# Performance work log

Measured on AMD Instinct MI355X. Metric: run time of the kernel, lower is better.

Reference implementation:

```python
import jax, jax.numpy as jnp
import numpy as np

N_NODES = 50000
NEG_SLOPE = 0.2


def gatv2_layer(x, src, dst, Wl, bl, Wr, br, att, bias, n_nodes):
    """GATv2Conv (PyG semantics, share_weights=False, concat=True).
    src/dst already include self-loops. att: [H, C]."""
    H, C = att.shape
    xl = (x @ Wl + bl).reshape(n_nodes, H, C)  # source transform
    xr = (x @ Wr + br).reshape(n_nodes, H, C)  # target transform
    # per-edge attention logits: att . LeakyReLU(xl[j] + xr[i])
    g = jax.nn.leaky_relu(xl[src] + xr[dst], NEG_SLOPE)      # [E,H,C]
    score = jnp.einsum('ehc,hc->eh', g, att)                  # [E,H]
    # segment softmax over incoming edges of each dst node
    m = jax.ops.segment_max(score, dst, num_segments=n_nodes)
    ex = jnp.exp(score - m[dst])
    denom = jax.ops.segment_sum(ex, dst, num_segments=n_nodes)
    alpha = ex / denom[dst]                                   # [E,H]
    out = jax.ops.segment_sum(alpha[:, :, None] * xl[src], dst, num_segments=n_nodes)
    return out.reshape(n_nodes, H * C) + bias


def setup_inputs() -> dict:
    key = jax.random.key(0)
    ks = jax.random.split(key, 20)
    N, IN, HID, H, OUT = N_NODES, 128, 64, 4, 64
    E, EL = 800000, 200000

    def w(k, shape, fan_in):
        return jax.random.normal(k, shape, jnp.float32) * (1.0 / np.sqrt(fan_in))

    inp = {
        'x': jax.random.normal(ks[0], (N, IN), jnp.float32),
        'edge_index': jax.random.randint(ks[1], (2, E), 0, N, jnp.int32),
        'edge_label_index': jax.random.randint(ks[2], (2, EL), 0, N, jnp.int32),
        # conv1: in -> hid, heads=4
        'W1l': w(ks[3], (IN, H * HID), IN), 'b1l': jnp.zeros((H * HID,), jnp.float32),
        'W1r': w(ks[4], (IN, H * HID), IN), 'b1r': jnp.zeros((H * HID,), jnp.float32),
        'att1': w(ks[5], (H, HID), HID),   'bias1': jnp.zeros((H * HID,), jnp.float32),
        # conv2: hid*heads -> out, heads=1
        'W2l': w(ks[6], (H * HID, OUT), H * HID), 'b2l': jnp.zeros((OUT,), jnp.float32),
        'W2r': w(ks[7], (H * HID, OUT), H * HID), 'b2r': jnp.zeros((OUT,), jnp.float32),
        'att2': w(ks[8], (1, OUT), OUT),          'bias2': jnp.zeros((OUT,), jnp.float32),
        # mlp decoder: 2*out -> hid -> 1
        'Wm1': w(ks[9], (2 * OUT, HID), 2 * OUT), 'bm1': jnp.zeros((HID,), jnp.float32),
        'Wm2': w(ks[10], (HID, 1), HID),          'bm2': jnp.zeros((1,), jnp.float32),
    }
    return inp


def reference(x, edge_index, edge_label_index,
              W1l, b1l, W1r, b1r, att1, bias1,
              W2l, b2l, W2r, b2r, att2, bias2,
              Wm1, bm1, Wm2, bm2):
    N = x.shape[0]
    # PyG GATv2Conv add_self_loops=True (default)
    loop = jnp.arange(N, dtype=edge_index.dtype)
    src = jnp.concatenate([edge_index[0], loop])
    dst = jnp.concatenate([edge_index[1], loop])

    z = gatv2_layer(x, src, dst, W1l, b1l, W1r, b1r, att1, bias1, N)
    z = jax.nn.relu(z)
    # dropout is identity in eval mode
    z = gatv2_layer(z, src, dst, W2l, b2l, W2r, b2r, att2, bias2, N)

    # decode: gather endpoints, concat, 2-layer MLP -> [EL]
    feat = jnp.concatenate([z[edge_label_index[0]], z[edge_label_index[1]]], axis=-1)
    h = jax.nn.relu(feat @ Wm1 + bm1)
    return (h @ Wm2 + bm2).reshape(-1)
```

## Files before the change

kernel.cpp:

```cpp
#include <hip/hip_runtime.h>
#include <hip/hip_bf16.h>

#define IN_DIM 128
#define HID    64
#define NH     4
#define F1     256
#define OUTD   64
#define NEG    0.2f
#define LOG2E  1.44269504088896f

#define EXP2F(x) __builtin_amdgcn_exp2f(x)

typedef __attribute__((ext_vector_type(8))) short bf16x8;
typedef __attribute__((ext_vector_type(4))) float f32x4;
typedef __attribute__((ext_vector_type(4))) unsigned short u16x4;

__device__ __forceinline__ float bf2f(unsigned short h) {
  return __uint_as_float((unsigned)h << 16);
}
__device__ __forceinline__ unsigned short f2bf(float f) {
  unsigned u = __float_as_uint(f);
  u += 0x7fffu + ((u >> 16) & 1u);
  return (unsigned short)(u >> 16);
}
__device__ __forceinline__ bf16x8 f2bf8(const float* p) {
  float4 lo = *(const float4*)p;
  float4 hi = *(const float4*)(p + 4);
  bf16x8 r;
  r[0] = (short)f2bf(lo.x); r[1] = (short)f2bf(lo.y);
  r[2] = (short)f2bf(lo.z); r[3] = (short)f2bf(lo.w);
  r[4] = (short)f2bf(hi.x); r[5] = (short)f2bf(hi.y);
  r[6] = (short)f2bf(hi.z); r[7] = (short)f2bf(hi.w);
  return r;
}

__global__ __launch_bounds__(256) void k_cvt_all(
    const float* __restrict__ x, unsigned short* __restrict__ xb, int NX8,
    const float* __restrict__ W1l, const float* __restrict__ W1r,
    const float* __restrict__ W2l, const float* __restrict__ W2r,
    const float* __restrict__ Wm1,
    unsigned short* __restrict__ Wt, unsigned short* __restrict__ Wt2,
    unsigned short* __restrict__ Wuv, int* __restrict__ cnt4, int N) {
  int idx = blockIdx.x * 256 + threadIdx.x;
  if (idx < NX8) {
    bf16x8 r = f2bf8(x + (size_t)idx * 8);
    *(bf16x8*)(xb + (size_t)idx * 8) = r;
    return;
  }
  int j0 = idx - NX8;
  if (j0 < 4 * N) cnt4[j0] = 0;
  if (j0 < 512 * IN_DIM) {
    int c = j0 >> 7, k = j0 & 127;
    float v = (c < F1) ? W1l[k * F1 + c] : W1r[k * F1 + (c - F1)];
    Wt[j0] = f2bf(v);
  } else if (j0 < 512 * IN_DIM + 128 * F1) {
    int j = j0 - 512 * IN_DIM;
    int c = j >> 8, k = j & 255;
    float v = (c < OUTD) ? W2l[k * OUTD + c] : W2r[k * OUTD + (c - OUTD)];
    Wt2[j] = f2bf(v);
  } else if (j0 < 512 * IN_DIM + 128 * F1 + 128 * OUTD) {
    int j = j0 - 512 * IN_DIM - 128 * F1;
    int c = j >> 6, k = j & 63;
    float v = (c < OUTD) ? Wm1[k * OUTD + c] : Wm1[(64 + k) * OUTD + (c - OUTD)];
    Wuv[j] = f2bf(v);
  }
}

#define LWS 132
__global__ __launch_bounds__(256) void k_gemm1_mfma(
    const unsigned short* __restrict__ xb, const unsigned short* __restrict__ Wt,
    const float* __restrict__ bl, const float* __restrict__ br,
    unsigned short* __restrict__ xlh, unsigned short* __restrict__ xrh,
    const int* __restrict__ ei, int E, int* __restrict__ cnt4,
    int* __restrict__ rank, int N) {
  __shared__ __align__(16) unsigned short lw[128 * LWS];
  int tid = threadIdx.x, lane = tid & 63, w = tid >> 6;
  int node0 = blockIdx.x * 64 + w * 16;
  int colbase = blockIdx.y * 128;
  int l16 = lane & 15, khi = lane >> 4;
  int koff = khi * 8;
  {
    const unsigned short* src = Wt + (size_t)colbase * IN_DIM;
#pragma unroll
    for (int it = 0; it < 8; it++) {
      int c = it * 256 + tid;
      int col = c >> 4, k8 = (c & 15) * 8;
      *(bf16x8*)(&lw[col * LWS + k8]) = *(const bf16x8*)(src + col * IN_DIM + k8);
    }
  }
  int arow = node0 + l16; if (arow >= N) arow = N - 1;
  const unsigned short* ap = xb + (size_t)arow * IN_DIM + koff;
  bf16x8 b0 = *(const bf16x8*)(ap);
  bf16x8 b1 = *(const bf16x8*)(ap + 32);
  bf16x8 b2 = *(const bf16x8*)(ap + 64);
  bf16x8 b3 = *(const bf16x8*)(ap + 96);
  {
    int gid = blockIdx.y * gridDim.x + blockIdx.x;
    int e = gid * 256 + tid;
    if (e < E) {
      int d = ei[E + e];
      rank[e] = atomicAdd(&cnt4[blockIdx.y * N + d], 1);
    }
  }
  __syncthreads();
  int node = node0 + l16;
  bool nok = node < N;
  bool isL = (colbase < F1);
  unsigned short* dst = isL ? xlh : xrh;
  const float* bias = isL ? bl : br;
  int cofs = isL ? colbase : (colbase - F1);
#pragma unroll
  for (int cp = 0; cp < 4; cp++) {
    int ct0 = cp * 2, ct1 = cp * 2 + 1;
    const unsigned short* wp0 = &lw[(ct0 * 16 + l16) * LWS + koff];
    const unsigned short* wp1 = &lw[(ct1 * 16 + l16) * LWS + koff];
    f32x4 a0 = {0.f, 0.f, 0.f, 0.f};
    f32x4 a1 = {0.f, 0.f, 0.f, 0.f};
    a0 = __builtin_amdgcn_mfma_f32_16x16x32_bf16(*(const bf16x8*)(wp0), b0, a0, 0, 0, 0);
    a1 = __builtin_amdgcn_mfma_f32_16x16x32_bf16(*(const bf16x8*)(wp1), b0, a1, 0, 0, 0);
    a0 = __builtin_amdgcn_mfma_f32_16x16x32_bf16(*(const bf16x8*)(wp0 + 32), b1, a0, 0, 0, 0);
    a1 = __builtin_amdgcn_mfma_f32_16x16x32_bf16(*(const bf16x8*)(wp1 + 32), b1, a1, 0, 0, 0);
    a0 = __builtin_amdgcn_mfma_f32_16x16x32_bf16(*(const bf16x8*)(wp0 + 64), b2, a0, 0, 0, 0);
    a1 = __builtin_amdgcn_mfma_f32_16x16x32_bf16(*(const bf16x8*)(wp1 + 64), b2, a1, 0, 0, 0);
    a0 = __builtin_amdgcn_mfma_f32_16x16x32_bf16(*(const bf16x8*)(wp0 + 96), b3, a0, 0, 0, 0);
    a1 = __builtin_amdgcn_mfma_f32_16x16x32_bf16(*(const bf16x8*)(wp1 + 96), b3, a1, 0, 0, 0);
    int lc0 = ct0 * 16 + khi * 4;
    int lc1 = ct1 * 16 + khi * 4;
    float4 bb0 = *(const float4*)(bias + cofs + lc0);
    float4 bb1 = *(const float4*)(bias + cofs + lc1);
    if (nok) {
      u16x4 o0, o1;
      o0[0] = f2bf(a0[0] + bb0.x); o0[1] = f2bf(a0[1] + bb0.y);
      o0[2] = f2bf(a0[2] + bb0.z); o0[3] = f2bf(a0[3] + bb0.w);
      o1[0] = f2bf(a1[0] + bb1.x); o1[1] = f2bf(a1[1] + bb1.y);
      o1[2] = f2bf(a1[2] + bb1.z); o1[3] = f2bf(a1[3] + bb1.w);
      __builtin_nontemporal_store(o0, (u16x4*)(dst + (size_t)node * F1 + cofs + lc0));
      __builtin_nontemporal_store(o1, (u16x4*)(dst + (size_t)node * F1 + cofs + lc1));
    }
  }
}

__global__ __launch_bounds__(256) void k_gemm2_mfma(
    const unsigned short* __restrict__ zh, const unsigned short* __restrict__ Wt2,
    const float* __restrict__ bl, const float* __restrict__ br,
    unsigned short* __restrict__ xl2h, unsigned short* __restrict__ xr2h, int N) {
  int tid = threadIdx.x, lane = tid & 63, w = tid >> 6;
  int node0 = blockIdx.x * 64 + w * 16;
  int l16 = lane & 15, khi = lane >> 4;
  int koff = khi * 8;
  int arow = node0 + l16; if (arow >= N) arow = N - 1;
  const unsigned short* zp = zh + (size_t)arow * F1 + koff;
  bf16x8 bfr[8];
#pragma unroll
  for (int t = 0; t < 8; t++) bfr[t] = *(const bf16x8*)(zp + 32 * t);
  int node = node0 + l16;
  bool nok = node < N;
#pragma unroll
  for (int half = 0; half < 2; half++) {
    const unsigned short* Wbase = Wt2 + (size_t)half * OUTD * F1;
    unsigned short* dst = half ? xr2h : xl2h;
    const float* bias = half ? br : bl;
#pragma unroll
    for (int ct = 0; ct < 4; ct++) {
      int wrow = ct * 16 + l16;
      const unsigned short* wp = Wbase + (size_t)wrow * F1 + koff;
      f32x4 acc = {0.f, 0.f, 0.f, 0.f};
#pragma unroll
      for (int t = 0; t < 8; t++)
        acc = __builtin_amdgcn_mfma_f32_16x16x32_bf16(
            *(const bf16x8*)(wp + 32 * t), bfr[t], acc, 0, 0, 0);
      int cbase = ct * 16 + khi * 4;
      float4 bb = *(const float4*)(bias + cbase);
      if (nok) {
        ushort4 o;
        o.x = f2bf(acc[0] + bb.x); o.y = f2bf(acc[1] + bb.y);
        o.z = f2bf(acc[2] + bb.z); o.w = f2bf(acc[3] + bb.w);
        *(ushort4*)(dst + (size_t)node * OUTD + cbase) = o;
      }
    }
  }
}

__global__ __launch_bounds__(256) void k_uv_mfma(
    const unsigned short* __restrict__ z2h, const unsigned short* __restrict__ Wuv,
    float* __restrict__ u, float* __restrict__ v, int N) {
  int tid = threadIdx.x, lane = tid & 63, w = tid >> 6;
  int node0 = blockIdx.x * 64 + w * 16;
  int half = blockIdx.y;
  int l16 = lane & 15, khi = lane >> 4;
  int koff = khi * 8;
  int arow = node0 + l16; if (arow >= N) arow = N - 1;
  const unsigned short* zp = z2h + (size_t)arow * OUTD + koff;
  bf16x8 b0 = *(const bf16x8*)(zp);
  bf16x8 b1 = *(const bf16x8*)(zp + 32);
  const unsigned short* Wbase = Wuv + (size_t)half * OUTD * OUTD;
  float* dst = half ? v : u;
  int node = node0 + l16;
  bool nok = node < N;
#pragma unroll
  for (int ct = 0; ct < 4; ct++) {
    int wrow = ct * 16 + l16;
    const unsigned short* wp = Wbase + (size_t)wrow * OUTD + koff;
    f32x4 acc = {0.f, 0.f, 0.f, 0.f};
    acc = __builtin_amdgcn_mfma_f32_16x16x32_bf16(*(const bf16x8*)(wp), b0, acc, 0, 0, 0);
    acc = __builtin_amdgcn_mfma_f32_16x16x32_bf16(*(const bf16x8*)(wp + 32), b1, acc, 0, 0, 0);
    int cbase = ct * 16 + khi * 4;
    if (nok) {
      float4 o;
      o.x = acc[0]; o.y = acc[1]; o.z = acc[2]; o.w = acc[3];
      *(float4*)(dst + (size_t)node * OUTD + cbase) = o;
    }
  }
}

__global__ __launch_bounds__(256) void k_scan1(
    const int* __restrict__ cnt4, int N, int* __restrict__ lps,
    int* __restrict__ blk_sum) {
  int t = threadIdx.x, lane = t & 63, wid = t >> 6;
  int base = blockIdx.x * 1024 + t * 4;
  int4 v = {0, 0, 0, 0};
#pragma unroll
  for (int y = 0; y < 4; y++) {
    const int* c = cnt4 + (size_t)y * N;
    if (base + 3 < N) {
      int4 cy = *(const int4*)(c + base);
      v.x += cy.x; v.y += cy.y; v.z += cy.z; v.w += cy.w;
    } else {
      if (base + 0 < N) v.x += c[base + 0];
      if (base + 1 < N) v.y += c[base + 1];
      if (base + 2 < N) v.z += c[base + 2];
      if (base + 3 < N) v.w += c[base + 3];
    }
  }
  int s = v.x + v.y + v.z + v.w;
  int inc = s;
#pragma unroll
  for (int off = 1; off < 64; off <<= 1) {
    int u = __shfl_up(inc, off, 64);
    if (lane >= off) inc += u;
  }
  __shared__ int wsum[4];
  if (lane == 63) wsum[wid] = inc;
  __syncthreads();
  int wofs = 0;
#pragma unroll
  for (int q = 0; q < 4; q++) if (q < wid) wofs += wsum[q];
  int excl = wofs + inc - s;
  int4 o;
  o.x = excl; o.y = excl + v.x; o.z = o.y + v.y; o.w = o.z + v.z;
  if (base + 3 < N) {
    *(int4*)(lps + base) = o;
  } else {
    if (base + 0 < N) lps[base + 0] = o.x;
    if (base + 1 < N) lps[base + 1] = o.y;
    if (base + 2 < N) lps[base + 2] = o.z;
    if (base + 3 < N) lps[base + 3] = o.w;
  }
  if (t == 255) blk_sum[blockIdx.x] = wofs + inc;
}

__global__ void k_scan2(int* __restrict__ blk, int nblk) {
  int lane = threadIdx.x;
  int v = (lane < nblk) ? blk[lane] : 0;
  int inc = v;
#pragma unroll
  for (int off = 1; off < 64; off <<= 1) {
    int u = __shfl_up(inc, off, 64);
    if (lane >= off) inc += u;
  }
  if (lane < nblk) blk[lane] = inc - v;
}

__global__ __launch_bounds__(256) void k_scan3(
    const int* __restrict__ lps, const int* __restrict__ blk_sum,
    int N, int E, int* __restrict__ row_start, int* __restrict__ cnt4) {
  int i = blockIdx.x * 256 + threadIdx.x;
  if (i < N) {
    int p = lps[i] + blk_sum[i >> 10];
    row_start[i] = p;
    int c0 = cnt4[i];
    int c1 = cnt4[(size_t)N + i];
    int c2 = cnt4[(size_t)2 * N + i];
    cnt4[i] = p;
    cnt4[(size_t)N + i] = p + c0;
    cnt4[(size_t)2 * N + i] = p + c0 + c1;
    cnt4[(size_t)3 * N + i] = p + c0 + c1 + c2;
  }
  if (i == 0) row_start[N] = E;
}

__global__ __launch_bounds__(256) void k_scatter(
    const int* __restrict__ ei, int E, int per, const int* __restrict__ cnt4,
    const int* __restrict__ rank, int* __restrict__ csr_src, int N) {
  int e4 = (blockIdx.x * 256 + threadIdx.x) * 4;
  if (e4 + 3 < E) {
    int4 s = *(const int4*)(ei + e4);
    int4 d = *(const int4*)(ei + E + e4);
    int4 r = *(const int4*)(rank + e4);
    int y0 = e4 / per, y1 = (e4 + 1) / per;
    int y2 = (e4 + 2) / per, y3 = (e4 + 3) / per;
    csr_src[cnt4[(size_t)y0 * N + d.x] + r.x] = s.x;
    csr_src[cnt4[(size_t)y1 * N + d.y] + r.y] = s.y;
    csr_src[cnt4[(size_t)y2 * N + d.z] + r.z] = s.z;
    csr_src[cnt4[(size_t)y3 * N + d.w] + r.w] = s.w;
  } else {
    for (int e = e4; e < E; e++)
      csr_src[cnt4[(size_t)(e / per) * N + ei[E + e]] + rank[e]] = ei[e];
  }
}

#define DPP_ADD(p, ctrl)                                                     \
  p += __int_as_float(__builtin_amdgcn_update_dpp(                           \
      0, __float_as_int(p), ctrl, 0xF, 0xF, true))
#define RED16(p)  { DPP_ADD(p, 0xB1); DPP_ADD(p, 0x4E);                      \
                    DPP_ADD(p, 0x124); DPP_ADD(p, 0x128); }

#define BF4(dst, h)                                \
  dst.x = bf2f(h.x); dst.y = bf2f(h.y);            \
  dst.z = bf2f(h.z); dst.w = bf2f(h.w);

#define DOTABS(p, xv)                                              \
  { float t;                                                       \
    t = xv.x + xri.x; p = fmaf(t, a6.x, p); p = fmaf(fabsf(t), a4b.x, p); \
    t = xv.y + xri.y; p = fmaf(t, a6.y, p); p = fmaf(fabsf(t), a4b.y, p); \
    t = xv.z + xri.z; p = fmaf(t, a6.z, p); p = fmaf(fabsf(t), a4b.z, p); \
    t = xv.w + xri.w; p = fmaf(t, a6.w, p); p = fmaf(fabsf(t), a4b.w, p); }

#define SETUP_A64(att, stride)                                     \
  float4 a6 = *(const float4*)((att) + (stride));                  \
  a6.x *= LOG2E; a6.y *= LOG2E; a6.z *= LOG2E; a6.w *= LOG2E;      \
  float4 a4b;                                                      \
  a4b.x = 0.4f * a6.x; a4b.y = 0.4f * a6.y;                        \
  a4b.z = 0.4f * a6.z; a4b.w = 0.4f * a6.w;                        \
  a6.x *= 0.6f; a6.y *= 0.6f; a6.z *= 0.6f; a6.w *= 0.6f;

__global__ __launch_bounds__(256) void k_fused1(
    const unsigned short* __restrict__ xlh, const unsigned short* __restrict__ xrh,
    const int* __restrict__ row_start, const int* __restrict__ csr_src,
    const float* __restrict__ att, const float* __restrict__ bias,
    unsigned short* __restrict__ zh, int N) {
  int tid = threadIdx.x, lane = tid & 63, w = tid >> 6;
  int i = blockIdx.x * 4 + w;
  if (i >= N) return;
  float4 xri;
  {
    ushort4 hr = *(const ushort4*)(xrh + (size_t)i * F1 + lane * 4);
    BF4(xri, hr);
  }
  SETUP_A64(att, lane * 4);
  float den;
  float4 acc;
  {
    ushort4 hh = *(const ushort4*)(xlh + (size_t)i * F1 + lane * 4);
    float4 xs; BF4(xs, hh);
    float p = 0.f;
    DOTABS(p, xs);
    RED16(p);
    float wt = EXP2F(p);
    den = wt;
    acc.x = wt * xs.x; acc.y = wt * xs.y;
    acc.z = wt * xs.z; acc.w = wt * xs.w;
  }
  int b = row_start[i], e = row_start[i + 1];
  int k = b;
  for (; k + 3 < e; k += 4) {
    int s0 = csr_src[k], s1 = csr_src[k + 1];
    int s2 = csr_src[k + 2], s3 = csr_src[k + 3];
    ushort4 h0 = *(const ushort4*)(xlh + (size_t)s0 * F1 + lane * 4);
    ushort4 h1 = *(const ushort4*)(xlh + (size_t)s1 * F1 + lane * 4);
    ushort4 h2 = *(const ushort4*)(xlh + (size_t)s2 * F1 + lane * 4);
    ushort4 h3 = *(const ushort4*)(xlh + (size_t)s3 * F1 + lane * 4);
    float4 x0, x1, x2, x3;
    BF4(x0, h0); BF4(x1, h1); BF4(x2, h2); BF4(x3, h3);
    float p0 = 0.f, p1 = 0.f, p2 = 0.f, p3 = 0.f;
    DOTABS(p0, x0); DOTABS(p1, x1); DOTABS(p2, x2); DOTABS(p3, x3);
    RED16(p0); RED16(p1); RED16(p2); RED16(p3);
    float w0 = EXP2F(p0), w1 = EXP2F(p1);
    float w2 = EXP2F(p2), w3 = EXP2F(p3);
    den += (w0 + w1) + (w2 + w3);
    acc.x += w0 * x0.x + w1 * x1.x + w2 * x2.x + w3 * x3.x;
    acc.y += w0 * x0.y + w1 * x1.y + w2 * x2.y + w3 * x3.y;
    acc.z += w0 * x0.z + w1 * x1.z + w2 * x2.z + w3 * x3.z;
    acc.w += w0 * x0.w + w1 * x1.w + w2 * x2.w + w3 * x3.w;
  }
  for (; k < e; k++) {
    int s = csr_src[k];
    ushort4 hh = *(const ushort4*)(xlh + (size_t)s * F1 + lane * 4);
    float4 xs;
    BF4(xs, hh);
    float p = 0.f;
    DOTABS(p, xs);
    RED16(p);
    float wt = EXP2F(p);
    den += wt;
    acc.x += wt * xs.x;
    acc.y += wt * xs.y;
    acc.z += wt * xs.z;
    acc.w += wt * xs.w;
  }
  float inv = 1.f / den;
  float4 bz = *(const float4*)(bias + lane * 4);
  ushort4 o;
  o.x = f2bf(fmaxf(acc.x * inv + bz.x, 0.f));
  o.y = f2bf(fmaxf(acc.y * inv + bz.y, 0.f));
  o.z = f2bf(fmaxf(acc.z * inv + bz.z, 0.f));
  o.w = f2bf(fmaxf(acc.w * inv + bz.w, 0.f));
  *(ushort4*)(zh + (size_t)i * F1 + lane * 4) = o;
}

__global__ __launch_bounds__(256) void k_fused2(
    const unsigned short* __restrict__ xlh, const unsigned short* __restrict__ xrh2,
    const int* __restrict__ row_start, const int* __restrict__ csr_src,
    const float* __restrict__ att, const float* __restrict__ bias,
    unsigned short* __restrict__ z2h, int N) {
  int tid = threadIdx.x, lane = tid & 63, w = tid >> 6;
  int i = blockIdx.x * 4 + w;
  if (i >= N) return;
  int g = lane >> 4, l16 = lane & 15;
  float4 xri;
  {
    ushort4 hr = *(const ushort4*)(xrh2 + (size_t)i * OUTD + l16 * 4);
    BF4(xri, hr);
  }
  SETUP_A64(att, l16 * 4);
  float den = 0.f;
  float4 acc = {0.f, 0.f, 0.f, 0.f};
  if (g == 0) {
    ushort4 hh = *(const ushort4*)(xlh + (size_t)i * OUTD + l16 * 4);
    float4 xs; BF4(xs, hh);
    float p = 0.f;
    DOTABS(p, xs);
    RED16(p);
    float wt = EXP2F(p);
    den = wt;
    acc.x = wt * xs.x; acc.y = wt * xs.y;
    acc.z = wt * xs.z; acc.w = wt * xs.w;
  }
  int b = row_start[i], e = row_start[i + 1];
  int k = b;
  for (; k + 15 < e; k += 16) {
    int ea = k + g, eb = k + 4 + g, ec = k + 8 + g, ed = k + 12 + g;
    int sa = csr_src[ea], sb = csr_src[eb], sc = csr_src[ec], sd = csr_src[ed];
    ushort4 ha = *(const ushort4*)(xlh + (size_t)sa * OUTD + l16 * 4);
    ushort4 hb = *(const ushort4*)(xlh + (size_t)sb * OUTD + l16 * 4);
    ushort4 hc = *(const ushort4*)(xlh + (size_t)sc * OUTD + l16 * 4);
    ushort4 hd = *(const ushort4*)(xlh + (size_t)sd * OUTD + l16 * 4);
    float4 xa, xb, xc, xd;
    BF4(xa, ha); BF4(xb, hb); BF4(xc, hc); BF4(xd, hd);
    float pa = 0.f, pb = 0.f, pc = 0.f, pd = 0.f;
    DOTABS(pa, xa); DOTABS(pb, xb); DOTABS(pc, xc); DOTABS(pd, xd);
    RED16(pa); RED16(pb); RED16(pc); RED16(pd);
    float wa = EXP2F(pa), wb = EXP2F(pb), wc = EXP2F(pc), wd = EXP2F(pd);
    den += (wa + wb) + (wc + wd);
    acc.x += (wa * xa.x + wb * xb.x) + (wc * xc.x + wd * xd.x);
    acc.y += (wa * xa.y + wb * xb.y) + (wc * xc.y + wd * xd.y);
    acc.z += (wa * xa.z + wb * xb.z) + (wc * xc.z + wd * xd.z);
    acc.w += (wa * xa.w + wb * xb.w) + (wc * xc.w + wd * xd.w);
  }
  for (; k < e; k += 8) {
    int ea = k + g, eb = k + 4 + g;
    int sa = csr_src[ea < e ? ea : (e - 1)];
    int sb = csr_src[eb < e ? eb : (e - 1)];
    ushort4 ha = *(const ushort4*)(xlh + (size_t)sa * OUTD + l16 * 4);
    ushort4 hb = *(const ushort4*)(xlh + (size_t)sb * OUTD + l16 * 4);
    float4 xa, xb;
    BF4(xa, ha); BF4(xb, hb);
    float pa = 0.f, pb = 0.f;
    DOTABS(pa, xa); DOTABS(pb, xb);
    RED16(pa); RED16(pb);
    float wa = (ea < e) ? EXP2F(pa) : 0.f;
    float wb = (eb < e) ? EXP2F(pb) : 0.f;
    den += wa + wb;
    acc.x += wa * xa.x + wb * xb.x;
    acc.y += wa * xa.y + wb * xb.y;
    acc.z += wa * xa.z + wb * xb.z;
    acc.w += wa * xa.w + wb * xb.w;
  }
#pragma unroll
  for (int off = 16; off <= 32; off <<= 1) {
    den   += __shfl_xor(den, off, 64);
    acc.x += __shfl_xor(acc.x, off, 64);
    acc.y += __shfl_xor(acc.y, off, 64);
    acc.z += __shfl_xor(acc.z, off, 64);
    acc.w += __shfl_xor(acc.w, off, 64);
  }
  if (g == 0) {
    float inv = 1.f / den;
    float4 bz = *(const float4*)(bias + l16 * 4);
    ushort4 o;
    o.x = f2bf(acc.x * inv + bz.x);
    o.y = f2bf(acc.y * inv + bz.y);
    o.z = f2bf(acc.z * inv + bz.z);
    o.w = f2bf(acc.w * inv + bz.w);
    *(ushort4*)(z2h + (size_t)i * OUTD + l16 * 4) = o;
  }
}

__global__ __launch_bounds__(256) void k_link(
    const float* __restrict__ u, const float* __restrict__ v,
    const int* __restrict__ eli, int EL,
    const float* __restrict__ bm1, const float* __restrict__ Wm2,
    const float* __restrict__ bm2, float* __restrict__ out) {
  int tid = threadIdx.x, lane = tid & 63, w = tid >> 6;
  int li = lane >> 4, c4 = (lane & 15) * 4;
  int l = (blockIdx.x * 4 + w) * 4 + li;
  if (l >= EL) return;
  int a = eli[l], b = eli[EL + l];
  float4 uu = *(const float4*)(u + (size_t)a * OUTD + c4);
  float4 vv = *(const float4*)(v + (size_t)b * OUTD + c4);
  float4 bb = *(const float4*)(bm1 + c4);
  float4 ww = *(const float4*)(Wm2 + c4);
  float p = fmaxf(uu.x + vv.x + bb.x, 0.f) * ww.x
          + fmaxf(uu.y + vv.y + bb.y, 0.f) * ww.y
          + fmaxf(uu.z + vv.z + bb.z, 0.f) * ww.z
          + fmaxf(uu.w + vv.w + bb.w, 0.f) * ww.w;
  RED16(p);
  if ((lane & 15) == 0) out[l] = p + bm2[0];
}

extern "C" void kernel_launch(void* const* d_in, const int* in_sizes, int n_in,
                              void* d_out, int out_size, void* d_ws, size_t ws_size,
                              hipStream_t stream) {
  const float* x     = (const float*)d_in[0];
  const int*   ei    = (const int*)d_in[1];
  const int*   eli   = (const int*)d_in[2];
  const float* W1l   = (const float*)d_in[3];
  const float* b1l   = (const float*)d_in[4];
  const float* W1r   = (const float*)d_in[5];
  const float* b1r   = (const float*)d_in[6];
  const float* att1  = (const float*)d_in[7];
  const float* bias1 = (const float*)d_in[8];
  const float* W2l   = (const float*)d_in[9];
  const float* b2l   = (const float*)d_in[10];
  const float* W2r   = (const float*)d_in[11];
  const float* b2r   = (const float*)d_in[12];
  const float* att2  = (const float*)d_in[13];
  const float* bias2 = (const float*)d_in[14];
  const float* Wm1   = (const float*)d_in[15];
  const float* bm1   = (const float*)d_in[16];
  const float* Wm2   = (const float*)d_in[17];
  const float* bm2   = (const float*)d_in[18];

  int N = in_sizes[0] / IN_DIM;
  int E = in_sizes[1] / 2;
  int EL = in_sizes[2] / 2;

  char* ws = (char*)d_ws;
  unsigned short* xlh  = (unsigned short*)(ws);
  unsigned short* xb   = (unsigned short*)(ws + 25600000);
  unsigned short* Wt   = (unsigned short*)(ws + 38400000);
  unsigned short* Wt2  = (unsigned short*)(ws + 39000000);
  unsigned short* Wuv  = (unsigned short*)(ws + 39200000);
  unsigned short* xrh  = (unsigned short*)(ws + 51200000);
  unsigned short* zh   = (unsigned short*)(ws + 76800000);
  int*   row_start = (int*)(ws + 102400000);
  int*   csr_src   = (int*)(ws + 103000000);
  int*   blk_sum   = (int*)(ws + 106300000);
  int*   rank      = (int*)(ws + 106400000);
  int*   cnt4      = (int*)(ws + 109700000);
  int*   lps       = (int*)(ws + 110600000);
  unsigned short* xl2h = (unsigned short*)(ws);
  unsigned short* xr2h = (unsigned short*)(ws + 12800000);
  unsigned short* z2h  = (unsigned short*)(ws + 25600000);
  float* u_buf     = (float*)(ws + 51200000);
  float* v_buf     = (float*)(ws + 64000000);

  int nblk = (N + 1023) / 1024;
  int NX8 = N * IN_DIM / 8;
  int gx = (N + 63) / 64;
  int per = gx * 256;
  int cvt_total = NX8 + 4 * N;

  k_cvt_all<<<(cvt_total + 255) / 256, 256, 0, stream>>>(
      x, xb, NX8, W1l, W1r, W2l, W2r, Wm1, Wt, Wt2, Wuv, cnt4, N);
  {
    dim3 g1(gx, 4);
    k_gemm1_mfma<<<g1, 256, 0, stream>>>(xb, Wt, b1l, b1r, xlh, xrh,
                                         ei, E, cnt4, rank, N);
  }
  k_scan1<<<nblk, 256, 0, stream>>>(cnt4, N, lps, blk_sum);
  k_scan2<<<1, 64, 0, stream>>>(blk_sum, nblk);
  k_scan3<<<(N + 255) / 256, 256, 0, stream>>>(lps, blk_sum, N, E,
                                               row_start, cnt4);
  k_scatter<<<(E / 4 + 255) / 256, 256, 0, stream>>>(ei, E, per, cnt4, rank,
                                                     csr_src, N);

  k_fused1<<<(N + 3) / 4, 256, 0, stream>>>(xlh, xrh, row_start, csr_src,
                                            att1, bias1, zh, N);
  k_gemm2_mfma<<<(N + 63) / 64, 256, 0, stream>>>(zh, Wt2, b2l, b2r,
                                                  xl2h, xr2h, N);
  k_fused2<<<(N + 3) / 4, 256, 0, stream>>>(xl2h, xr2h, row_start, csr_src,
                                            att2, bias2, z2h, N);
  {
    dim3 g3((N + 63) / 64, 2);
    k_uv_mfma<<<g3, 256, 0, stream>>>(z2h, Wuv, u_buf, v_buf, N);
  }
  k_link<<<(EL + 15) / 16, 256, 0, stream>>>(u_buf, v_buf, eli, EL,
                                             bm1, Wm2, bm2, (float*)d_out);
}
```

Baseline: 250.6 us.

## Split layer-1 aggregation wave into two half-waves processing different edges with 16-byte loads

```diff
diff --git a/kernel.cpp b/kernel.cpp
--- a/kernel.cpp
+++ b/kernel.cpp
@@ -14,6 +14,7 @@
 typedef __attribute__((ext_vector_type(8))) short bf16x8;
 typedef __attribute__((ext_vector_type(4))) float f32x4;
 typedef __attribute__((ext_vector_type(4))) unsigned short u16x4;
+typedef __attribute__((ext_vector_type(8))) unsigned short u16x8;
 
 __device__ __forceinline__ float bf2f(unsigned short h) {
   return __uint_as_float((unsigned)h << 16);
@@ -314,10 +315,15 @@
       0, __float_as_int(p), ctrl, 0xF, 0xF, true))
 #define RED16(p)  { DPP_ADD(p, 0xB1); DPP_ADD(p, 0x4E);                      \
                     DPP_ADD(p, 0x124); DPP_ADD(p, 0x128); }
+#define RED8(p)   { DPP_ADD(p, 0xB1); DPP_ADD(p, 0x4E); DPP_ADD(p, 0x141); }
 
 #define BF4(dst, h)                                \
   dst.x = bf2f(h.x); dst.y = bf2f(h.y);            \
   dst.z = bf2f(h.z); dst.w = bf2f(h.w);
+
+#define BF8(dA, dB, h)                                                       \
+  dA.x = bf2f(h[0]); dA.y = bf2f(h[1]); dA.z = bf2f(h[2]); dA.w = bf2f(h[3]);\
+  dB.x = bf2f(h[4]); dB.y = bf2f(h[5]); dB.z = bf2f(h[6]); dB.w = bf2f(h[7]);
 
 #define DOTABS(p, xv)                                              \
   { float t;                                                       \
@@ -325,6 +331,17 @@
     t = xv.y + xri.y; p = fmaf(t, a6.y, p); p = fmaf(fabsf(t), a4b.y, p); \
     t = xv.z + xri.z; p = fmaf(t, a6.z, p); p = fmaf(fabsf(t), a4b.z, p); \
     t = xv.w + xri.w; p = fmaf(t, a6.w, p); p = fmaf(fabsf(t), a4b.w, p); }
+
+#define DOT8(p, xvA, xvB)                                          \
+  { float t;                                                       \
+    t = xvA.x + xriA.x; p = fmaf(t, a6A.x, p); p = fmaf(fabsf(t), a4bA.x, p); \
+    t = xvA.y + xriA.y; p = fmaf(t, a6A.y, p); p = fmaf(fabsf(t), a4bA.y, p); \
+    t = xvA.z + xriA.z; p = fmaf(t, a6A.z, p); p = fmaf(fabsf(t), a4bA.z, p); \
+    t = xvA.w + xriA.w; p = fmaf(t, a6A.w, p); p = fmaf(fabsf(t), a4bA.w, p); \
+    t = xvB.x + xriB.x; p = fmaf(t, a6B.x, p); p = fmaf(fabsf(t), a4bB.x, p); \
+    t = xvB.y + xriB.y; p = fmaf(t, a6B.y, p); p = fmaf(fabsf(t), a4bB.y, p); \
+    t = xvB.z + xriB.z; p = fmaf(t, a6B.z, p); p = fmaf(fabsf(t), a4bB.z, p); \
+    t = xvB.w + xriB.w; p = fmaf(t, a6B.w, p); p = fmaf(fabsf(t), a4bB.w, p); }
 
 #define SETUP_A64(att, stride)                                     \
   float4 a6 = *(const float4*)((att) + (stride));                  \
@@ -333,6 +350,19 @@
   a4b.x = 0.4f * a6.x; a4b.y = 0.4f * a6.y;                        \
   a4b.z = 0.4f * a6.z; a4b.w = 0.4f * a6.w;                        \
   a6.x *= 0.6f; a6.y *= 0.6f; a6.z *= 0.6f; a6.w *= 0.6f;
+
+#define SETUP_A8(att, stride)                                      \
+  float4 a6A = *(const float4*)((att) + (stride));                 \
+  float4 a6B = *(const float4*)((att) + (stride) + 4);             \
+  a6A.x *= LOG2E; a6A.y *= LOG2E; a6A.z *= LOG2E; a6A.w *= LOG2E;  \
+  a6B.x *= LOG2E; a6B.y *= LOG2E; a6B.z *= LOG2E; a6B.w *= LOG2E;  \
+  float4 a4bA, a4bB;                                               \
+  a4bA.x = 0.4f * a6A.x; a4bA.y = 0.4f * a6A.y;                    \
+  a4bA.z = 0.4f * a6A.z; a4bA.w = 0.4f * a6A.w;                    \
+  a4bB.x = 0.4f * a6B.x; a4bB.y = 0.4f * a6B.y;                    \
+  a4bB.z = 0.4f * a6B.z; a4bB.w = 0.4f * a6B.w;                    \
+  a6A.x *= 0.6f; a6A.y *= 0.6f; a6A.z *= 0.6f; a6A.w *= 0.6f;      \
+  a6B.x *= 0.6f; a6B.y *= 0.6f; a6B.z *= 0.6f; a6B.w *= 0.6f;
 
 __global__ __launch_bounds__(256) void k_fused1(
     const unsigned short* __restrict__ xlh, const unsigned short* __restrict__ xrh,
@@ -342,70 +372,84 @@
   int tid = threadIdx.x, lane = tid & 63, w = tid >> 6;
   int i = blockIdx.x * 4 + w;
   if (i >= N) return;
-  float4 xri;
+  int g2 = lane >> 5, l32 = lane & 31;
+  int ch = l32 * 8;
+  float4 xriA, xriB;
   {
-    ushort4 hr = *(const ushort4*)(xrh + (size_t)i * F1 + lane * 4);
-    BF4(xri, hr);
-  }
-  SETUP_A64(att, lane * 4);
-  float den;
-  float4 acc;
-  {
-    ushort4 hh = *(const ushort4*)(xlh + (size_t)i * F1 + lane * 4);
-    float4 xs; BF4(xs, hh);
+    bf16x8 hr = *(const bf16x8*)(xrh + (size_t)i * F1 + ch);
+    BF8(xriA, xriB, hr);
+  }
+  SETUP_A8(att, ch);
+  float den = 0.f;
+  float4 accA = {0.f, 0.f, 0.f, 0.f};
+  float4 accB = {0.f, 0.f, 0.f, 0.f};
+  int b = row_start[i], e = row_start[i + 1];
+  int L = e - b + 1;
+  int j = 0;
+  for (; j + 3 < L; j += 4) {
+    int idx0 = j + g2;
+    int s0 = (idx0 > 0) ? csr_src[b + idx0 - 1] : i;
+    int s1 = csr_src[b + j + 1 + g2];
+    bf16x8 h0 = *(const bf16x8*)(xlh + (size_t)s0 * F1 + ch);
+    bf16x8 h1 = *(const bf16x8*)(xlh + (size_t)s1 * F1 + ch);
+    float4 x0A, x0B, x1A, x1B;
+    BF8(x0A, x0B, h0); BF8(x1A, x1B, h1);
+    float p0 = 0.f, p1 = 0.f;
+    DOT8(p0, x0A, x0B); DOT8(p1, x1A, x1B);
+    RED8(p0); RED8(p1);
+    float w0 = EXP2F(p0), w1 = EXP2F(p1);
+    den += w0 + w1;
+    accA.x += w0 * x0A.x + w1 * x1A.x;
+    accA.y += w0 * x0A.y + w1 * x1A.y;
+    accA.z += w0 * x0A.z + w1 * x1A.z;
+    accA.w += w0 * x0A.w + w1 * x1A.w;
+    accB.x += w0 * x0B.x + w1 * x1B.x;
+    accB.y += w0 * x0B.y + w1 * x1B.y;
+    accB.z += w0 * x0B.z + w1 * x1B.z;
+    accB.w += w0 * x0B.w + w1 * x1B.w;
+  }
+  for (; j < L; j += 2) {
+    int idx = j + g2;
+    bool act = idx < L;
+    int s = i;
+    if (act && idx > 0) s = csr_src[b + idx - 1];
+    bf16x8 h = *(const bf16x8*)(xlh + (size_t)s * F1 + ch);
+    float4 xA, xB;
+    BF8(xA, xB, h);
     float p = 0.f;
-    DOTABS(p, xs);
-    RED16(p);
-    float wt = EXP2F(p);
-    den = wt;
-    acc.x = wt * xs.x; acc.y = wt * xs.y;
-    acc.z = wt * xs.z; acc.w = wt * xs.w;
-  }
-  int b = row_start[i], e = row_start[i + 1];
-  int k = b;
-  for (; k + 3 < e; k += 4) {
-    int s0 = csr_src[k], s1 = csr_src[k + 1];
-    int s2 = csr_src[k + 2], s3 = csr_src[k + 3];
-    ushort4 h0 = *(const ushort4*)(xlh + (size_t)s0 * F1 + lane * 4);
-    ushort4 h1 = *(const ushort4*)(xlh + (size_t)s1 * F1 + lane * 4);
-    ushort4 h2 = *(const ushort4*)(xlh + (size_t)s2 * F1 + lane * 4);
-    ushort4 h3 = *(const ushort4*)(xlh + (size_t)s3 * F1 + lane * 4);
-    float4 x0, x1, x2, x3;
-    BF4(x0, h0); BF4(x1, h1); BF4(x2, h2); BF4(x3, h3);
-    float p0 = 0.f, p1 = 0.f, p2 = 0.f, p3 = 0.f;
-    DOTABS(p0, x0); DOTABS(p1, x1); DOTABS(p2, x2); DOTABS(p3, x3);
-    RED16(p0); RED16(p1); RED16(p2); RED16(p3);
-    float w0 = EXP2F(p0), w1 = EXP2F(p1);
-    float w2 = EXP2F(p2), w3 = EXP2F(p3);
-    den += (w0 + w1) + (w2 + w3);
-    acc.x += w0 * x0.x + w1 * x1.x + w2 * x2.x + w3 * x3.x;
-    acc.y += w0 * x0.y + w1 * x1.y + w2 * x2.y + w3 * x3.y;
-    acc.z += w0 * x0.z + w1 * x1.z + w2 * x2.z + w3 * x3.z;
-    acc.w += w0 * x0.w + w1 * x1.w + w2 * x2.w + w3 * x3.w;
-  }
-  for (; k < e; k++) {
-    int s = csr_src[k];
-    ushort4 hh = *(const ushort4*)(xlh + (size_t)s * F1 + lane * 4);
-    float4 xs;
-    BF4(xs, hh);
-    float p = 0.f;
-    DOTABS(p, xs);
-    RED16(p);
-    float wt = EXP2F(p);
+    DOT8(p, xA, xB);
+    RED8(p);
+    float wt = act ? EXP2F(p) : 0.f;
     den += wt;
-    acc.x += wt * xs.x;
-    acc.y += wt * xs.y;
-    acc.z += wt * xs.z;
-    acc.w += wt * xs.w;
-  }
-  float inv = 1.f / den;
-  float4 bz = *(const float4*)(bias + lane * 4);
-  ushort4 o;
-  o.x = f2bf(fmaxf(acc.x * inv + bz.x, 0.f));
-  o.y = f2bf(fmaxf(acc.y * inv + bz.y, 0.f));
-  o.z = f2bf(fmaxf(acc.z * inv + bz.z, 0.f));
-  o.w = f2bf(fmaxf(acc.w * inv + bz.w, 0.f));
-  *(ushort4*)(zh + (size_t)i * F1 + lane * 4) = o;
+    accA.x += wt * xA.x; accA.y += wt * xA.y;
+    accA.z += wt * xA.z; accA.w += wt * xA.w;
+    accB.x += wt * xB.x; accB.y += wt * xB.y;
+    accB.z += wt * xB.z; accB.w += wt * xB.w;
+  }
+  den   += __shfl_xor(den, 32, 64);
+  accA.x += __shfl_xor(accA.x, 32, 64);
+  accA.y += __shfl_xor(accA.y, 32, 64);
+  accA.z += __shfl_xor(accA.z, 32, 64);
+  accA.w += __shfl_xor(accA.w, 32, 64);
+  accB.x += __shfl_xor(accB.x, 32, 64);
+  accB.y += __shfl_xor(accB.y, 32, 64);
+  accB.z += __shfl_xor(accB.z, 32, 64);
+  accB.w += __shfl_xor(accB.w, 32, 64);
+  if (g2 == 0) {
+    float inv = 1.f / den;
+    float4 bzA = *(const float4*)(bias + ch);
+    float4 bzB = *(const float4*)(bias + ch + 4);
+    u16x8 o;
+    o[0] = f2bf(fmaxf(accA.x * inv + bzA.x, 0.f));
+    o[1] = f2bf(fmaxf(accA.y * inv + bzA.y, 0.f));
+    o[2] = f2bf(fmaxf(accA.z * inv + bzA.z, 0.f));
+    o[3] = f2bf(fmaxf(accA.w * inv + bzA.w, 0.f));
+    o[4] = f2bf(fmaxf(accB.x * inv + bzB.x, 0.f));
+    o[5] = f2bf(fmaxf(accB.y * inv + bzB.y, 0.f));
+    o[6] = f2bf(fmaxf(accB.z * inv + bzB.z, 0.f));
+    o[7] = f2bf(fmaxf(accB.w * inv + bzB.w, 0.f));
+    *(u16x8*)(zh + (size_t)i * F1 + ch) = o;
+  }
 }
 
 __global__ __launch_bounds__(256) void k_fused2(
```

After: 250.7 us. About the same (+0.0%).
